# Kernel tuning notes

Measured on AMD Instinct MI355X. Metric: run time of the kernel, lower is better.

The kernel has to match this reference:

```python
import jax, jax.numpy as jnp
import numpy as np

N = 50000   # nodes
H = 4       # heads
R = 3       # relations
E = 524288  # edges per relation


def _gatv2_rel(x, Wsrc, Wdst, a, src, dst, n_heads):
    """Single-relation GATv2: returns [N, H, D] aggregated messages."""
    hs = (x @ Wsrc).reshape(x.shape[0], n_heads, -1)  # [N,H,D]
    hd = (x @ Wdst).reshape(x.shape[0], n_heads, -1)  # [N,H,D]
    m = hs[src] + hd[dst]                              # [E,H,D] gather
    e = jnp.einsum('ehd,hd->eh', jax.nn.leaky_relu(m, 0.2), a)  # [E,H]
    # segment softmax over incoming edges of each destination node
    emax = jax.ops.segment_max(e, dst, num_segments=N)          # [N,H]
    ee = jnp.exp(e - emax[dst])
    den = jax.ops.segment_sum(ee, dst, num_segments=N)          # [N,H]
    alpha = ee / (den[dst] + 1e-9)                              # [E,H]
    msg = alpha[..., None] * hs[src]                            # [E,H,D]
    return jax.ops.segment_sum(msg, dst, num_segments=N)        # [N,H,D]


def setup_inputs() -> dict:
    key = jax.random.key(0)
    ks = jax.random.split(key, 9)
    sc = lambda f: 1.0 / np.sqrt(f)
    return {
        'x': jax.random.normal(ks[0], (N, 128), jnp.float32),
        'src': jax.random.randint(ks[1], (R, E), 0, N, jnp.int32),
        'dst': jax.random.randint(ks[2], (R, E), 0, N, jnp.int32),
        'W1_src': jax.random.normal(ks[3], (R, 128, 128), jnp.float32) * sc(128),
        'W1_dst': jax.random.normal(ks[4], (R, 128, 128), jnp.float32) * sc(128),
        'a1': jax.random.normal(ks[5], (R, H, 32), jnp.float32) * sc(32),
        'W2_src': jax.random.normal(ks[6], (R, 128, 256), jnp.float32) * sc(128),
        'W2_dst': jax.random.normal(ks[7], (R, 128, 256), jnp.float32) * sc(128),
        'a2': jax.random.normal(ks[8], (R, H, 64), jnp.float32) * sc(64),
    }


def reference(x, src, dst, W1_src, W1_dst, a1, W2_src, W2_dst, a2):
    # Layer 1: sum GATv2 over relations, relu, flatten heads -> [N, hid]
    h = jnp.zeros((N, H, 32), x.dtype)
    for r in range(R):
        h = h + _gatv2_rel(x, W1_src[r], W1_dst[r], a1[r], src[r], dst[r], H)
    h = jax.nn.relu(h).reshape(N, H * 32)  # [N, 128]
    # Layer 2: sum GATv2 over relations -> [N, H, out]
    out = jnp.zeros((N, H, 64), x.dtype)
    for r in range(R):
        out = out + _gatv2_rel(h, W2_src[r], W2_dst[r], a2[r], src[r], dst[r], H)
    return out
```

## Files before the change

### kernel.cpp

```cpp
#include <hip/hip_runtime.h>
#include <hip/hip_bf16.h>

#define NN 50000
#define HH 4
#define RR 3
#define EE 524288
#define ESHIFT 19
#define TN (RR*NN)
#define NCHUNK ((TN + 1023)/1024)
#define LOG2E 1.4426950408889634f

typedef __attribute__((ext_vector_type(8))) short short8;
typedef __attribute__((ext_vector_type(4))) short short4v;
typedef __attribute__((ext_vector_type(4))) float float4v;
typedef __attribute__((ext_vector_type(2))) float float2v;
typedef __attribute__((ext_vector_type(2))) _Float16 half2v;

#if defined(__has_builtin)
#if __has_builtin(__builtin_amdgcn_fdot2)
#define USE_FDOT2 1
#else
#define USE_FDOT2 0
#endif
#else
#define USE_FDOT2 0
#endif


__device__ inline void tw_body(const float* __restrict__ W, __hip_bfloat16* __restrict__ T,
                               int ncs, int colOff, int i) {
    int r = i >> (7 + ncs);
    int rem = i & ((128 << ncs) - 1);
    int k = rem >> ncs;
    int n = rem & ((1 << ncs) - 1);
    T[(size_t)((r << (1 + ncs)) + colOff + n) * 128 + k] = __float2bfloat16(W[i]);
}

__launch_bounds__(256)
__global__ void prep_kernel(const float* __restrict__ x, short4v* __restrict__ xb,
                            const float* __restrict__ W1s, const float* __restrict__ W1d,
                            const float* __restrict__ W2s, const float* __restrict__ W2d,
                            __hip_bfloat16* __restrict__ T1, __hip_bfloat16* __restrict__ T2,
                            const int* __restrict__ dst, int* __restrict__ deg) {
    int wg = blockIdx.x, t = threadIdx.x;
    if (wg < 6250) {
        int i = wg * 256 + t;
        float4v v = ((const float4v*)x)[i];
        short4v o;
        o.x = (short)__bfloat16_as_ushort(__float2bfloat16(v.x));
        o.y = (short)__bfloat16_as_ushort(__float2bfloat16(v.y));
        o.z = (short)__bfloat16_as_ushort(__float2bfloat16(v.z));
        o.w = (short)__bfloat16_as_ushort(__float2bfloat16(v.w));
        xb[i] = o;
    } else if (wg < 6442) {
        tw_body(W1s, T1, 7, 0, (wg - 6250) * 256 + t);
    } else if (wg < 6634) {
        tw_body(W1d, T1, 7, 128, (wg - 6442) * 256 + t);
    } else if (wg < 7018) {
        tw_body(W2s, T2, 8, 0, (wg - 6634) * 256 + t);
    } else if (wg < 7402) {
        tw_body(W2d, T2, 8, 256, (wg - 7018) * 256 + t);
    } else {
        int i = (wg - 7402) * 256 + t;
        int r = i >> ESHIFT;
        atomicAdd(&deg[r * NN + dst[i]], 1);
    }
}


__global__ void scan1_kernel(const int* __restrict__ deg, int* __restrict__ part) {
    __shared__ int s[256];
    int t = threadIdx.x;
    int base = blockIdx.x * 1024 + t * 4;
    int sum = 0;
#pragma unroll
    for (int j = 0; j < 4; j++) {
        int idx = base + j;
        sum += (idx < TN) ? deg[idx] : 0;
    }
    s[t] = sum;
    __syncthreads();
    for (int off = 128; off > 0; off >>= 1) {
        if (t < off) s[t] += s[t + off];
        __syncthreads();
    }
    if (t == 0) part[blockIdx.x] = s[0];
}

__global__ void scan2_kernel(int* part) {
    int run = 0;
    for (int i = 0; i < NCHUNK; i++) {
        int v = part[i];
        part[i] = run;
        run += v;
    }
}

__global__ void scan3_kernel(const int* __restrict__ deg, const int* __restrict__ part,
                             int* __restrict__ offs, int* __restrict__ curs) {
    __shared__ int s[256];
    int t = threadIdx.x;
    int base = blockIdx.x * 1024 + t * 4;
    int v[4];
    int tsum = 0;
#pragma unroll
    for (int j = 0; j < 4; j++) {
        int idx = base + j;
        v[j] = (idx < TN) ? deg[idx] : 0;
        tsum += v[j];
    }
    s[t] = tsum;
    __syncthreads();
    for (int off = 1; off < 256; off <<= 1) {
        int x = (t >= off) ? s[t - off] : 0;
        __syncthreads();
        s[t] += x;
        __syncthreads();
    }
    int excl = s[t] - tsum + part[blockIdx.x];
    int run = excl;
#pragma unroll
    for (int j = 0; j < 4; j++) {
        int idx = base + j;
        if (idx < TN) {
            offs[idx] = run;
            curs[idx] = run;
            run += v[j];
        }
    }
}


__device__ inline void gemm_body(const __hip_bfloat16* __restrict__ A,
                                 const __hip_bfloat16* __restrict__ Bt,
                                 _Float16* __restrict__ C,
                                 int M, int nshift, int tile_m, int tn0, int tn1, int t) {
    __shared__ __hip_bfloat16 Bs[64 * 136];
    int w = t >> 6, lane = t & 63;
    int m16 = lane & 15, quad = lane >> 4;
    int row = tile_m + w * 16 + m16;
    int rowc = row < M ? row : M - 1;

    short8 a[4];
    const short8* ap = (const short8*)(A + (size_t)rowc * 128);
#pragma unroll
    for (int kf = 0; kf < 4; kf++) a[kf] = ap[quad + kf * 4];

    int cmask = (1 << nshift) - 1;

    for (int tn = tn0; tn < tn1; ++tn) {
        int tile_n = tn * 64;
        {
            const uint4* gsrc = (const uint4*)(Bt + (size_t)tile_n * 128);
#pragma unroll
            for (int e = t; e < 64 * 16; e += 256) {
                int n = e >> 4, c = e & 15;
                uint4 val = gsrc[n * 16 + c];
                *(uint4*)(&Bs[n * 136 + c * 8]) = val;
            }
        }
        __syncthreads();

        float4v acc[4];
#pragma unroll
        for (int ct = 0; ct < 4; ct++) {
            acc[ct] = (float4v){0.f, 0.f, 0.f, 0.f};
            const short8* bp = (const short8*)(Bs + (ct * 16 + m16) * 136);
#pragma unroll
            for (int kf = 0; kf < 4; kf++) {
                short8 b = bp[quad + kf * 4];
                acc[ct] = __builtin_amdgcn_mfma_f32_16x16x32_bf16(a[kf], b, acc[ct], 0, 0, 0);
            }
        }
        __syncthreads();

#pragma unroll
        for (int ct = 0; ct < 4; ct++) {
            int col = tile_n + ct * 16 + m16;
            int tbl = col >> nshift;
            int cc = col & cmask;
            size_t base = ((size_t)tbl * M) << nshift;
#pragma unroll
            for (int rg = 0; rg < 4; rg++) {
                int rr = tile_m + w * 16 + quad * 4 + rg;
                if (rr < M) C[base + (((size_t)rr) << nshift) + cc] = (_Float16)acc[ct][rg];
            }
        }
    }
}

__launch_bounds__(256)
__global__ void gemm_kernel(const __hip_bfloat16* __restrict__ A,
                            const __hip_bfloat16* __restrict__ Bt,
                            _Float16* __restrict__ C,
                            int M, int nshift, int tilesPerSplit) {
    gemm_body(A, Bt, C, M, nshift, blockIdx.x * 64,
              blockIdx.y * tilesPerSplit, blockIdx.y * tilesPerSplit + tilesPerSplit,
              threadIdx.x);
}


__launch_bounds__(256)
__global__ void work1_kernel(const __hip_bfloat16* __restrict__ A,
                             const __hip_bfloat16* __restrict__ Bt,
                             _Float16* __restrict__ C,
                             const int* __restrict__ src, const int* __restrict__ dst,
                             int* __restrict__ curs, int* __restrict__ esrc) {
    int wg = blockIdx.x;
    if (wg < 2346) {
        int gx = wg % 782;
        int gy = wg / 782;
        gemm_body(A, Bt, C, NN, 7, gx * 64, gy * 4, gy * 4 + 4, threadIdx.x);
    } else {
        int wg2 = wg - 2346;
        int p = wg2 / 6144;
        int i = (wg2 - p * 6144) * 256 + threadIdx.x;
        int d = dst[i];
        if ((unsigned)(d - p * 12500) < 12500u) {
            int r = i >> ESHIFT;
            int pos = atomicAdd(&curs[r * NN + d], 1);
            esrc[pos] = src[i] << 8;
        }
    }
}


template <int W2>
__device__ inline void ldrow16(const char* __restrict__ p, half2v* hv) {
    if constexpr (W2 == 2) {
        uint2 pk = *(const uint2*)p;
        hv[0] = __builtin_bit_cast(half2v, pk.x);
        hv[1] = __builtin_bit_cast(half2v, pk.y);
    } else {
        uint4 pk = *(const uint4*)p;
        hv[0] = __builtin_bit_cast(half2v, pk.x);
        hv[1] = __builtin_bit_cast(half2v, pk.y);
        hv[2] = __builtin_bit_cast(half2v, pk.z);
        hv[3] = __builtin_bit_cast(half2v, pk.w);
    }
}

template <int W2>
__device__ inline float edot16(const half2v* hv, const half2v* hdv, const half2v* al) {
    const half2v c02 = {(_Float16)0.2f, (_Float16)0.2f};
    float s = 0.f;
#pragma unroll
    for (int j = 0; j < W2; j++) {
        half2v m = hv[j] + hdv[j];
        half2v lr = __builtin_elementwise_max(m, m * c02);
#if USE_FDOT2
        s = __builtin_amdgcn_fdot2(lr, al[j], s, false);
#else
        half2v tt = lr * al[j];
        s += (float)tt.x + (float)tt.y;
#endif
    }
    return s;
}

template <int CTRL>
__device__ inline float dpp_add(float s) {
    int t = __builtin_amdgcn_update_dpp(0, __float_as_int(s), CTRL, 0xF, 0xF, true);
    return s + __int_as_float(t);
}

__device__ inline float hred8(float s) {
    s = dpp_add<0xB1>(s);
    s = dpp_add<0x4E>(s);
    s = dpp_add<0x141>(s);
    return s;
}

template <int W2, bool L1, int SH>
__launch_bounds__(256)
__global__ void agg_kernel(const char* __restrict__ C,
                           const float* __restrict__ a,
                           const int* __restrict__ offs, const int* __restrict__ deg,
                           const int* __restrict__ esrc,
                           float* __restrict__ outf, __hip_bfloat16* __restrict__ outb) {
    const int V = 2 * W2;
    const int NC = 32 * V;
    const int ROWB = NC * 2;
    int wid = (blockIdx.x * 256 + threadIdx.x) >> 6;
    int lane = threadIdx.x & 63;
    int g = lane >> 5;
    int c = lane & 31;
    int eb = c * V;
    int ebb = eb * 2;
    int kb = g << 1;

    float2v total[W2];
#pragma unroll
    for (int j = 0; j < W2; j++) total[j] = (float2v){0.f, 0.f};

#pragma unroll 1
    for (int r = 0; r < RR; r++) {
        const char* hsb = C + (size_t)(2 * r) * NN * ROWB + ebb;
        const char* hdb = C + (size_t)(2 * r + 1) * NN * ROWB + ebb;
        half2v hdv[W2], al[W2];
        float2v acc[W2];
        ldrow16<W2>(hdb + (size_t)wid * ROWB, hdv);
#pragma unroll
        for (int j = 0; j < W2; j++) {
            al[j] = (half2v){(_Float16)(a[r * NC + eb + 2 * j] * LOG2E),
                             (_Float16)(a[r * NC + eb + 2 * j + 1] * LOG2E)};
            acc[j] = (float2v){0.f, 0.f};
        }
        float den = 0.f;
        int e0 = offs[r * NN + wid];
        int dg = deg[r * NN + wid];
        int elast = e0 + ((dg > 0) ? dg : 1) - 1;
        int nfull = dg >> 3;
        int rem = dg & 7;
        int u0 = esrc[min(e0 + kb,     elast)];
        int u1 = esrc[min(e0 + kb + 1, elast)];
        int u2 = esrc[min(e0 + kb + 4, elast)];
        int u3 = esrc[min(e0 + kb + 5, elast)];
        for (int it = 0; it < nfull; ++it) {
            int kn = (it << 3) + 8;
            int n0 = esrc[min(e0 + kn + kb,     elast)];
            int n1 = esrc[min(e0 + kn + kb + 1, elast)];
            int n2 = esrc[min(e0 + kn + kb + 4, elast)];
            int n3 = esrc[min(e0 + kn + kb + 5, elast)];
            half2v hv0[W2], hv1[W2], hv2[W2], hv3[W2];
            ldrow16<W2>(hsb + ((size_t)(unsigned)u0 << SH), hv0);
            ldrow16<W2>(hsb + ((size_t)(unsigned)u1 << SH), hv1);
            ldrow16<W2>(hsb + ((size_t)(unsigned)u2 << SH), hv2);
            ldrow16<W2>(hsb + ((size_t)(unsigned)u3 << SH), hv3);
            float p0 = __builtin_amdgcn_exp2f(hred8(edot16<W2>(hv0, hdv, al)));
            float p1 = __builtin_amdgcn_exp2f(hred8(edot16<W2>(hv1, hdv, al)));
            float p2 = __builtin_amdgcn_exp2f(hred8(edot16<W2>(hv2, hdv, al)));
            float p3 = __builtin_amdgcn_exp2f(hred8(edot16<W2>(hv3, hdv, al)));
            den += (p0 + p1) + (p2 + p3);
#pragma unroll
            for (int j = 0; j < W2; j++) {
                acc[j].x = __builtin_fmaf(p0, (float)hv0[j].x, acc[j].x);
                acc[j].y = __builtin_fmaf(p0, (float)hv0[j].y, acc[j].y);
                acc[j].x = __builtin_fmaf(p1, (float)hv1[j].x, acc[j].x);
                acc[j].y = __builtin_fmaf(p1, (float)hv1[j].y, acc[j].y);
                acc[j].x = __builtin_fmaf(p2, (float)hv2[j].x, acc[j].x);
                acc[j].y = __builtin_fmaf(p2, (float)hv2[j].y, acc[j].y);
                acc[j].x = __builtin_fmaf(p3, (float)hv3[j].x, acc[j].x);
                acc[j].y = __builtin_fmaf(p3, (float)hv3[j].y, acc[j].y);
            }
            u0 = n0; u1 = n1; u2 = n2; u3 = n3;
        }
        if (rem) {
            if (rem <= 4) {
                half2v hv0[W2], hv1[W2];
                ldrow16<W2>(hsb + ((size_t)(unsigned)u0 << SH), hv0);
                ldrow16<W2>(hsb + ((size_t)(unsigned)u1 << SH), hv1);
                float s0 = hred8(edot16<W2>(hv0, hdv, al));
                float s1 = hred8(edot16<W2>(hv1, hdv, al));
                float p0 = (kb     < rem) ? __builtin_amdgcn_exp2f(s0) : 0.f;
                float p1 = (kb + 1 < rem) ? __builtin_amdgcn_exp2f(s1) : 0.f;
                den += p0 + p1;
#pragma unroll
                for (int j = 0; j < W2; j++) {
                    acc[j].x = __builtin_fmaf(p0, (float)hv0[j].x, acc[j].x);
                    acc[j].y = __builtin_fmaf(p0, (float)hv0[j].y, acc[j].y);
                    acc[j].x = __builtin_fmaf(p1, (float)hv1[j].x, acc[j].x);
                    acc[j].y = __builtin_fmaf(p1, (float)hv1[j].y, acc[j].y);
                }
            } else {
                half2v hv0[W2], hv1[W2], hv2[W2], hv3[W2];
                ldrow16<W2>(hsb + ((size_t)(unsigned)u0 << SH), hv0);
                ldrow16<W2>(hsb + ((size_t)(unsigned)u1 << SH), hv1);
                ldrow16<W2>(hsb + ((size_t)(unsigned)u2 << SH), hv2);
                ldrow16<W2>(hsb + ((size_t)(unsigned)u3 << SH), hv3);
                float s0 = hred8(edot16<W2>(hv0, hdv, al));
                float s1 = hred8(edot16<W2>(hv1, hdv, al));
                float s2 = hred8(edot16<W2>(hv2, hdv, al));
                float s3 = hred8(edot16<W2>(hv3, hdv, al));
                float p0 = (kb     < rem) ? __builtin_amdgcn_exp2f(s0) : 0.f;
                float p1 = (kb + 1 < rem) ? __builtin_amdgcn_exp2f(s1) : 0.f;
                float p2 = (kb + 4 < rem) ? __builtin_amdgcn_exp2f(s2) : 0.f;
                float p3 = (kb + 5 < rem) ? __builtin_amdgcn_exp2f(s3) : 0.f;
                den += (p0 + p1) + (p2 + p3);
#pragma unroll
                for (int j = 0; j < W2; j++) {
                    acc[j].x = __builtin_fmaf(p0, (float)hv0[j].x, acc[j].x);
                    acc[j].y = __builtin_fmaf(p0, (float)hv0[j].y, acc[j].y);
                    acc[j].x = __builtin_fmaf(p1, (float)hv1[j].x, acc[j].x);
                    acc[j].y = __builtin_fmaf(p1, (float)hv1[j].y, acc[j].y);
                    acc[j].x = __builtin_fmaf(p2, (float)hv2[j].x, acc[j].x);
                    acc[j].y = __builtin_fmaf(p2, (float)hv2[j].y, acc[j].y);
                    acc[j].x = __builtin_fmaf(p3, (float)hv3[j].x, acc[j].x);
                    acc[j].y = __builtin_fmaf(p3, (float)hv3[j].y, acc[j].y);
                }
            }
        }
        den += __shfl_xor(den, 32);
        float inv = 1.f / (den + 1e-9f);
        float2v iv = (float2v){inv, inv};
#pragma unroll
        for (int j = 0; j < W2; j++) {
            float2v tt = acc[j];
            tt.x += __shfl_xor(tt.x, 32);
            tt.y += __shfl_xor(tt.y, 32);
            total[j] += tt * iv;
        }
    }

    if (g == 0) {
        if constexpr (L1) {
#pragma unroll
            for (int j = 0; j < W2; j++) {
                float v0 = total[j].x, v1 = total[j].y;
                outb[(size_t)wid * NC + eb + 2 * j]     = __float2bfloat16(v0 > 0.f ? v0 : 0.f);
                outb[(size_t)wid * NC + eb + 2 * j + 1] = __float2bfloat16(v1 > 0.f ? v1 : 0.f);
            }
        } else {
#pragma unroll
            for (int j = 0; j < W2; j++) {
                outf[(size_t)wid * NC + eb + 2 * j]     = total[j].x;
                outf[(size_t)wid * NC + eb + 2 * j + 1] = total[j].y;
            }
        }
    }
}


extern "C" void kernel_launch(void* const* d_in, const int* in_sizes, int n_in,
                              void* d_out, int out_size, void* d_ws, size_t ws_size,
                              hipStream_t stream) {
    const float* x   = (const float*)d_in[0];
    const int*   src = (const int*)d_in[1];
    const int*   dst = (const int*)d_in[2];
    const float* W1s = (const float*)d_in[3];
    const float* W1d = (const float*)d_in[4];
    const float* a1  = (const float*)d_in[5];
    const float* W2s = (const float*)d_in[6];
    const float* W2d = (const float*)d_in[7];
    const float* a2  = (const float*)d_in[8];

    char* ws = (char*)d_ws;
    size_t off = 0;
    auto alloc = [&](size_t bytes) -> void* {
        void* p = ws + off;
        off += (bytes + 255) & ~(size_t)255;
        return p;
    };
    __hip_bfloat16* xb = (__hip_bfloat16*)alloc((size_t)NN * 128 * 2);
    __hip_bfloat16* hb = (__hip_bfloat16*)alloc((size_t)NN * 128 * 2);
    _Float16*       Cb = (_Float16*)alloc((size_t)NN * 1536 * 2);
    __hip_bfloat16* T1 = (__hip_bfloat16*)alloc((size_t)768 * 128 * 2);
    __hip_bfloat16* T2 = (__hip_bfloat16*)alloc((size_t)1536 * 128 * 2);
    int* deg  = (int*)alloc((size_t)TN * 4);
    int* offs = (int*)alloc((size_t)TN * 4);
    int* curs = (int*)alloc((size_t)TN * 4);
    int* esrc = (int*)alloc((size_t)RR * EE * 4);
    int* part = (int*)alloc(4096);

    float* outp = (float*)d_out;

    hipMemsetAsync(deg, 0, (size_t)TN * 4, stream);

    prep_kernel<<<13546, 256, 0, stream>>>(x, (short4v*)xb, W1s, W1d, W2s, W2d,
                                           T1, T2, dst, deg);

    scan1_kernel<<<NCHUNK, 256, 0, stream>>>(deg, part);
    scan2_kernel<<<1, 1, 0, stream>>>(part);
    scan3_kernel<<<NCHUNK, 256, 0, stream>>>(deg, part, offs, curs);

    work1_kernel<<<2346 + 24576, 256, 0, stream>>>(xb, T1, Cb, src, dst, curs, esrc);

    agg_kernel<2, true, 0><<<12500, 256, 0, stream>>>((const char*)Cb, a1, offs, deg, esrc,
                                                      nullptr, hb);

    gemm_kernel<<<dim3(782, 4), 256, 0, stream>>>(hb, T2, Cb, NN, 8, 6);

    agg_kernel<4, false, 1><<<12500, 256, 0, stream>>>((const char*)Cb, a2, offs, deg, esrc,
                                                       outp, nullptr);
}
```

Baseline: 509.3 us.

## Overlap layer-2 GEMM on first node half with layer-1 aggregation of second half

Splits the layer-1 aggregation into two node ranges and changes the layer-1 buffer layout so its tables sit in the upper half of each doubled-stride slot. A fused work2 kernel runs the layer-2 GEMM for the first 24960 nodes alongside aggregation of the remaining nodes, and a trailing GEMM handles the rest. The aim is to fill the GPU while the memory-bound aggregation runs, at the cost of a more complex buffer layout and an extra launch.

Measured after the change: 529.2 us. 3.9% more time.

```diff
diff --git a/kernel.cpp b/kernel.cpp
--- a/kernel.cpp
+++ b/kernel.cpp
@@ -9,6 +9,8 @@
 #define TN (RR*NN)
 #define NCHUNK ((TN + 1023)/1024)
 #define LOG2E 1.4426950408889634f
+
+#define SPLIT 24960
 
 typedef __attribute__((ext_vector_type(8))) short short8;
 typedef __attribute__((ext_vector_type(4))) short short4v;
@@ -134,7 +136,8 @@
 __device__ inline void gemm_body(const __hip_bfloat16* __restrict__ A,
                                  const __hip_bfloat16* __restrict__ Bt,
                                  _Float16* __restrict__ C,
-                                 int M, int nshift, int tile_m, int tn0, int tn1, int t) {
+                                 int M, int nshift, int tile_m, int tn0, int tn1, int t,
+                                 size_t tblStride, size_t tblOff) {
     __shared__ __hip_bfloat16 Bs[64 * 136];
     int w = t >> 6, lane = t & 63;
     int m16 = lane & 15, quad = lane >> 4;
@@ -179,7 +182,7 @@
             int col = tile_n + ct * 16 + m16;
             int tbl = col >> nshift;
             int cc = col & cmask;
-            size_t base = ((size_t)tbl * M) << nshift;
+            size_t base = (size_t)tbl * tblStride + tblOff;
 #pragma unroll
             for (int rg = 0; rg < 4; rg++) {
                 int rr = tile_m + w * 16 + quad * 4 + rg;
@@ -193,10 +196,11 @@
 __global__ void gemm_kernel(const __hip_bfloat16* __restrict__ A,
                             const __hip_bfloat16* __restrict__ Bt,
                             _Float16* __restrict__ C,
-                            int M, int nshift, int tilesPerSplit) {
-    gemm_body(A, Bt, C, M, nshift, blockIdx.x * 64,
+                            int M, int nshift, int tilesPerSplit, int tmBase,
+                            size_t tblStride, size_t tblOff) {
+    gemm_body(A, Bt, C, M, nshift, (tmBase + blockIdx.x) * 64,
               blockIdx.y * tilesPerSplit, blockIdx.y * tilesPerSplit + tilesPerSplit,
-              threadIdx.x);
+              threadIdx.x, tblStride, tblOff);
 }
 
 
@@ -210,7 +214,8 @@
     if (wg < 2346) {
         int gx = wg % 782;
         int gy = wg / 782;
-        gemm_body(A, Bt, C, NN, 7, gx * 64, gy * 4, gy * 4 + 4, threadIdx.x);
+        gemm_body(A, Bt, C, NN, 7, gx * 64, gy * 4, gy * 4 + 4, threadIdx.x,
+                  (size_t)NN << 8, (size_t)NN << 7);
     } else {
         int wg2 = wg - 2346;
         int p = wg2 / 6144;
@@ -272,22 +277,21 @@
 }
 
 template <int W2, bool L1, int SH>
-__launch_bounds__(256)
-__global__ void agg_kernel(const char* __restrict__ C,
-                           const float* __restrict__ a,
-                           const int* __restrict__ offs, const int* __restrict__ deg,
-                           const int* __restrict__ esrc,
-                           float* __restrict__ outf, __hip_bfloat16* __restrict__ outb) {
+__device__ inline void agg_body(const char* __restrict__ C, const float* __restrict__ a,
+                                const int* __restrict__ offs, const int* __restrict__ deg,
+                                const int* __restrict__ esrc,
+                                float* __restrict__ outf, __hip_bfloat16* __restrict__ outb,
+                                int blockId, int widBase, size_t tstride, size_t toff) {
     const int V = 2 * W2;
     const int NC = 32 * V;
-    const int ROWB = NC * 2;
-    int wid = (blockIdx.x * 256 + threadIdx.x) >> 6;
+    int wid = widBase + ((blockId * 256 + (int)threadIdx.x) >> 6);
     int lane = threadIdx.x & 63;
     int g = lane >> 5;
     int c = lane & 31;
     int eb = c * V;
     int ebb = eb * 2;
     int kb = g << 1;
+    const size_t ROWB = (size_t)NC * 2;
 
     float2v total[W2];
 #pragma unroll
@@ -295,8 +299,8 @@
 
 #pragma unroll 1
     for (int r = 0; r < RR; r++) {
-        const char* hsb = C + (size_t)(2 * r) * NN * ROWB + ebb;
-        const char* hdb = C + (size_t)(2 * r + 1) * NN * ROWB + ebb;
+        const char* hsb = C + (size_t)(2 * r) * tstride + toff + ebb;
+        const char* hdb = C + (size_t)(2 * r + 1) * tstride + toff + ebb;
         half2v hdv[W2], al[W2];
         float2v acc[W2];
         ldrow16<W2>(hdb + (size_t)wid * ROWB, hdv);
@@ -420,6 +424,37 @@
     }
 }
 
+template <int W2, bool L1, int SH>
+__launch_bounds__(256)
+__global__ void agg_kernel(const char* __restrict__ C, const float* __restrict__ a,
+                           const int* __restrict__ offs, const int* __restrict__ deg,
+                           const int* __restrict__ esrc,
+                           float* __restrict__ outf, __hip_bfloat16* __restrict__ outb,
+                           int widBase, size_t tstride, size_t toff) {
+    agg_body<W2, L1, SH>(C, a, offs, deg, esrc, outf, outb, blockIdx.x, widBase, tstride, toff);
+}
+
+
+__launch_bounds__(256)
+__global__ void work2_kernel(const __hip_bfloat16* __restrict__ hb,
+                             const __hip_bfloat16* __restrict__ T2,
+                             _Float16* __restrict__ Cb,
+                             const char* __restrict__ C1, const float* __restrict__ a1,
+                             const int* __restrict__ offs, const int* __restrict__ deg,
+                             const int* __restrict__ esrc,
+                             __hip_bfloat16* __restrict__ hbout) {
+    int wg = blockIdx.x;
+    if (wg < 1560) {
+        int gx = wg % 390;
+        int gy = wg / 390;
+        gemm_body(hb, T2, Cb, NN, 8, gx * 64, gy * 6, gy * 6 + 6, threadIdx.x,
+                  (size_t)NN << 8, 0);
+    } else {
+        agg_body<2, true, 0>(C1, a1, offs, deg, esrc, nullptr, hbout,
+                             wg - 1560, SPLIT, (size_t)NN * 512, (size_t)NN * 256);
+    }
+}
+
 
 extern "C" void kernel_launch(void* const* d_in, const int* in_sizes, int n_in,
                               void* d_out, int out_size, void* d_ws, size_t ws_size,
@@ -465,11 +500,17 @@
 
     work1_kernel<<<2346 + 24576, 256, 0, stream>>>(xb, T1, Cb, src, dst, curs, esrc);
 
-    agg_kernel<2, true, 0><<<12500, 256, 0, stream>>>((const char*)Cb, a1, offs, deg, esrc,
-                                                      nullptr, hb);
-
-    gemm_kernel<<<dim3(782, 4), 256, 0, stream>>>(hb, T2, Cb, NN, 8, 6);
+    agg_kernel<2, true, 0><<<6240, 256, 0, stream>>>((const char*)Cb, a1, offs, deg, esrc,
+                                                     nullptr, hb, 0,
+                                                     (size_t)NN * 512, (size_t)NN * 256);
+
+    work2_kernel<<<1560 + 6260, 256, 0, stream>>>(hb, T2, Cb, (const char*)Cb, a1,
+                                                  offs, deg, esrc, hb);
+
+    gemm_kernel<<<dim3(392, 4), 256, 0, stream>>>(hb, T2, Cb, NN, 8, 6, 390,
+                                                  (size_t)NN << 8, 0);
 
     agg_kernel<4, false, 1><<<12500, 256, 0, stream>>>((const char*)Cb, a2, offs, deg, esrc,
-                                                       outp, nullptr);
-}
+                                                       outp, nullptr, 0,
+                                                       (size_t)NN * 512, 0);
+}
```
